# Optimization experiments

Measured on AMD Instinct MI355X. Metric: run time of the kernel, lower is better.

Reference implementation:

```python
import jax, jax.numpy as jnp
import numpy as np

B, P, F = 128, 196, 2048   # batch, num_pixels, feature_dim
E, H, V = 512, 512, 10000  # embed_dim, hidden_dim, vocab_size
T = 32                     # max caption length


def setup_inputs() -> dict:
    key = jax.random.key(0)
    ks = jax.random.split(key, 12)
    s_e, s_h, s_f = 1.0 / np.sqrt(E), 1.0 / np.sqrt(H), 1.0 / np.sqrt(F)
    return {
        "features": jax.random.normal(ks[0], (B, P, F), jnp.float32),
        "captions": jax.random.randint(ks[1], (B, T), 0, V),
        # embedding table (init uniform(-0.1, 0.1) in the original)
        "emb_W": jax.random.uniform(ks[2], (V, E), jnp.float32, -0.1, 0.1),
        # LSTMCell params (PyTorch layout: [4H, in] with gate order i,f,g,o)
        "W_ih": jax.random.uniform(ks[3], (4 * H, E), jnp.float32, -s_h, s_h),
        "W_hh": jax.random.uniform(ks[4], (4 * H, H), jnp.float32, -s_h, s_h),
        "b_ih": jax.random.uniform(ks[5], (4 * H,), jnp.float32, -s_h, s_h),
        "b_hh": jax.random.uniform(ks[6], (4 * H,), jnp.float32, -s_h, s_h),
        # init_h / init_c linear layers: feature_dim -> hidden_dim
        "Wh": jax.random.uniform(ks[7], (H, F), jnp.float32, -s_f, s_f),
        "bh": jax.random.uniform(ks[8], (H,), jnp.float32, -s_f, s_f),
        "Wc": jax.random.uniform(ks[9], (H, F), jnp.float32, -s_f, s_f),
        "bc": jax.random.uniform(ks[10], (H,), jnp.float32, -s_f, s_f),
        # output projection (uniform(-0.1, 0.1) weights, zero bias)
        "fc_W": jax.random.uniform(ks[11], (V, H), jnp.float32, -0.1, 0.1),
        "fc_b": jnp.zeros((V,), jnp.float32),
    }


def _decode(features, captions, emb_W, W_ih, W_hh, b_ih, b_hh, Wh, bh, Wc, bc, fc_W, fc_b):
    # init hidden state from mean pooled features
    mean_feat = features.mean(axis=1)                       # [B, F]
    h0 = mean_feat @ Wh.T + bh                              # [B, H]
    c0 = mean_feat @ Wc.T + bc                              # [B, H]

    embeds = emb_W[captions]                                # [B, T, E]
    # x-side gate preactivations for all steps at once: [T-1, B, 4H]
    x_gates = jnp.einsum('bte,ge->tbg', embeds[:, :-1, :], W_ih) + (b_ih + b_hh)

    def step(carry, xg):
        h, c = carry
        gates = xg + h @ W_hh.T                             # [B, 4H]
        i, f, g, o = jnp.split(gates, 4, axis=-1)
        i, f, o = jax.nn.sigmoid(i), jax.nn.sigmoid(f), jax.nn.sigmoid(o)
        g = jnp.tanh(g)
        c_new = f * c + i * g
        h_new = o * jnp.tanh(c_new)
        return (h_new, c_new), h_new

    _, hs = jax.lax.scan(step, (h0, c0), x_gates)           # hs: [T-1, B, H]
    hs = jnp.swapaxes(hs, 0, 1)                             # [B, T-1, H]
    # dropout is identity in eval mode; fc applied per step == batched matmul
    return jnp.einsum('bth,vh->btv', hs, fc_W) + fc_b       # [B, T-1, V]


def reference(features, captions, emb_W, W_ih, W_hh, b_ih, b_hh, Wh, bh, Wc, bc, fc_W, fc_b):
    return _decode(features, captions, emb_W, W_ih, W_hh, b_ih, b_hh, Wh, bh, Wc, bc, fc_W, fc_b)
```

## Files before the change

### kernel.cpp

```cpp
#include <hip/hip_runtime.h>
#include <hip/hip_bf16.h>
#include <cstddef>

#define Bz 128
#define Pz 196
#define Fz 2048
#define Ez 512
#define Hz 512
#define Vz 10000
#define Tz 32
#define TM 31
#define Mrows (Bz * TM)
#define MPAD 4096
#define G4 (4 * Hz)
#define NPAD 10240

typedef __attribute__((ext_vector_type(8))) short bf16x8;
typedef __attribute__((ext_vector_type(4))) float f32x4;

__device__ __forceinline__ void gload_lds16(const void* g, void* l) {
    __builtin_amdgcn_global_load_lds(
        (const __attribute__((address_space(1))) unsigned int*)g,
        (__attribute__((address_space(3))) unsigned int*)l, 16, 0, 0);
}
__device__ __forceinline__ ushort f2b(float x) {
    __hip_bfloat16 b = __float2bfloat16(x);
    return *reinterpret_cast<ushort*>(&b);
}
__device__ __forceinline__ float b2f(ushort u) {
    __hip_bfloat16 b = *reinterpret_cast<__hip_bfloat16*>(&u);
    return __bfloat162float(b);
}

__global__ __launch_bounds__(256) void meanpool(const float* __restrict__ feat,
                                                float* __restrict__ mean) {
    int idx = blockIdx.x * 256 + threadIdx.x;
    int b = idx >> 9;
    int q = idx & 511;
    const float4* base = reinterpret_cast<const float4*>(feat) +
                         (size_t)b * Pz * (Fz / 4) + q;
    float4 acc = {0.f, 0.f, 0.f, 0.f};
    for (int p = 0; p < Pz; ++p) {
        float4 v = base[(size_t)p * (Fz / 4)];
        acc.x += v.x; acc.y += v.y; acc.z += v.z; acc.w += v.w;
    }
    const float s = 1.0f / (float)Pz;
    acc.x *= s; acc.y *= s; acc.z *= s; acc.w *= s;
    reinterpret_cast<float4*>(mean)[idx] = acc;
}

#define PR0 (Mrows * 128)
#define PR1 (PR0 + 2 * G4 * 128)
#define PR2 (PR1 + NPAD * 128)
__global__ __launch_bounds__(256) void prep_all(
    const float* __restrict__ emb,  const int* __restrict__ cap,
    const float* __restrict__ Wih,  const float* __restrict__ Whh,
    const float* __restrict__ b1,   const float* __restrict__ b2,
    const float* __restrict__ fcW,
    ushort* __restrict__ embg, ushort* __restrict__ WihP,
    ushort* __restrict__ WhhP, float* __restrict__ bP,
    ushort* __restrict__ fcWb)
{
    int idx = blockIdx.x * 256 + threadIdx.x;
    if (idx < PR0) {
        int m = idx >> 7, kq = idx & 127;
        int b = m / TM;
        int t = m - b * TM;
        int row = cap[b * Tz + t];
        float4 v = reinterpret_cast<const float4*>(emb + (size_t)row * Ez)[kq];
        ushort4 o = {f2b(v.x), f2b(v.y), f2b(v.z), f2b(v.w)};
        reinterpret_cast<ushort4*>(embg + (size_t)m * Ez)[kq] = o;
    } else if (idx < PR1) {
        int rem = idx - PR0;
        int sel = rem >> 18;
        rem &= (1 << 18) - 1;
        int o = rem >> 7, kq = rem & 127;
        int j = o >> 2, g = o & 3;
        int in = g * Hz + j;
        if (sel == 0) {
            float4 v = reinterpret_cast<const float4*>(Wih + (size_t)in * Ez)[kq];
            ushort4 u = {f2b(v.x), f2b(v.y), f2b(v.z), f2b(v.w)};
            reinterpret_cast<ushort4*>(WihP + (size_t)o * Ez)[kq] = u;
            if (kq == 0) bP[o] = b1[in] + b2[in];
        } else {
            float4 v = reinterpret_cast<const float4*>(Whh + (size_t)in * Hz)[kq];
            ushort4 u = {f2b(v.x), f2b(v.y), f2b(v.z), f2b(v.w)};
            reinterpret_cast<ushort4*>(WhhP + (size_t)o * Hz)[kq] = u;
        }
    } else if (idx < PR2) {
        int i = idx - PR1;
        ushort4 o;
        if (i < Vz * Hz / 4) {
            float4 v = reinterpret_cast<const float4*>(fcW)[i];
            o.x = f2b(v.x); o.y = f2b(v.y); o.z = f2b(v.z); o.w = f2b(v.w);
        } else {
            o.x = o.y = o.z = o.w = 0;
        }
        reinterpret_cast<ushort4*>(fcWb)[i] = o;
    }
}

__global__ __launch_bounds__(256) void initk(
    const float* __restrict__ mean,
    const float* __restrict__ Wh, const float* __restrict__ Wc,
    float* __restrict__ partial)
{
    __shared__ float As[64][33];
    __shared__ float Bs2[64][33];
    const int n0 = blockIdx.x * 64;
    const int m0 = blockIdx.y * 64;
    const int kz = blockIdx.z;
    const int tid = threadIdx.x;
    const int tx = tid & 15, ty = tid >> 4;
    float acc[4][4] = {};

    for (int k0 = kz * 256; k0 < kz * 256 + 256; k0 += 32) {
#pragma unroll
        for (int i = 0; i < 2; ++i) {
            int e  = tid + i * 256;
            int r  = e >> 3;
            int cc = (e & 7) << 2;
            float4 va = *reinterpret_cast<const float4*>(
                mean + (size_t)(m0 + r) * Fz + k0 + cc);
            As[r][cc + 0] = va.x; As[r][cc + 1] = va.y;
            As[r][cc + 2] = va.z; As[r][cc + 3] = va.w;
            int n = n0 + r;
            const float* Brow = (n < Hz) ? (Wh + (size_t)n * Fz)
                                         : (Wc + (size_t)(n - Hz) * Fz);
            float4 vb = *reinterpret_cast<const float4*>(Brow + k0 + cc);
            Bs2[r][cc + 0] = vb.x; Bs2[r][cc + 1] = vb.y;
            Bs2[r][cc + 2] = vb.z; Bs2[r][cc + 3] = vb.w;
        }
        __syncthreads();
#pragma unroll
        for (int kk = 0; kk < 32; ++kk) {
            float a[4], bb[4];
#pragma unroll
            for (int i = 0; i < 4; ++i) a[i] = As[ty * 4 + i][kk];
#pragma unroll
            for (int j = 0; j < 4; ++j) bb[j] = Bs2[tx * 4 + j][kk];
#pragma unroll
            for (int i = 0; i < 4; ++i)
#pragma unroll
                for (int j = 0; j < 4; ++j)
                    acc[i][j] += a[i] * bb[j];
        }
        __syncthreads();
    }
#pragma unroll
    for (int i = 0; i < 4; ++i)
#pragma unroll
        for (int j = 0; j < 4; ++j)
            partial[((size_t)kz * 128 + m0 + ty * 4 + i) * 1024 + n0 + tx * 4 + j]
                = acc[i][j];
}

__global__ __launch_bounds__(256) void init_reduce(
    const float* __restrict__ partial,
    const float* __restrict__ bh, const float* __restrict__ bc,
    ushort* __restrict__ haHi, ushort* __restrict__ haLo,
    float* __restrict__ c0f)
{
    int idx = blockIdx.x * 256 + threadIdx.x;
    if (idx >= 128 * 1024) return;
    int m = idx >> 10, n = idx & 1023;
    float s = 0.f;
#pragma unroll
    for (int z = 0; z < 8; ++z)
        s += partial[((size_t)z * 128 + m) * 1024 + n];
    if (n < Hz) {
        s += bh[n];
        ushort hh = f2b(s);
        haHi[(size_t)m * Hz + n] = hh;
        haLo[(size_t)m * Hz + n] = f2b(s - b2f(hh));
    } else {
        c0f[(size_t)m * Hz + (n - Hz)] = s + bc[n - Hz];
    }
}

__global__ __launch_bounds__(256) void gemm_mfma(
    const ushort* __restrict__ A,
    const ushort* __restrict__ B,
    const float* __restrict__ bias,
    float* __restrict__ C,
    int Nb, int ldc, int K)
{
    __shared__ short Al[2][128 * 32];
    __shared__ short Bl[2][128 * 32];
    const int tid  = threadIdx.x;
    const int w    = tid >> 6;
    const int lane = tid & 63;

    const int nwg  = gridDim.x * gridDim.y;
    int orig = blockIdx.y * gridDim.x + blockIdx.x;
    int q = nwg >> 3, r = nwg & 7;
    int xcd = orig & 7, local = orig >> 3;
    int wgid = (xcd < r ? xcd * (q + 1) : r * (q + 1) + (xcd - r) * q) + local;
    const int m0 = (wgid / gridDim.x) * 128;
    const int n0 = (wgid % gridDim.x) * 128;
    const int wr = w >> 1, wc = w & 1;

    f32x4 acc[4][4] = {};

    const int srow = w * 32 + (lane >> 2);
    const int scol = (lane & 3) * 16;
    const char* Ag = (const char*)(A + (size_t)(m0 + srow) * K) + scol;
    const char* Bg = (const char*)(B + (size_t)(n0 + srow) * K) + scol;
    const size_t rstep = (size_t)16 * K * 2;
    const int ldsb = (w * 32) * 32;

    const int ko = (lane >> 4) * 8;
    const int fr = lane & 15;
    const int nk = K >> 5;

    gload_lds16(Ag,         Al[0] + ldsb);
    gload_lds16(Ag + rstep, Al[0] + ldsb + 16 * 32);
    gload_lds16(Bg,         Bl[0] + ldsb);
    gload_lds16(Bg + rstep, Bl[0] + ldsb + 16 * 32);
    __syncthreads();

    int cur = 0;
    for (int k = 0; k < nk; ++k) {
        if (k + 1 < nk) {
            const size_t kb = (size_t)(k + 1) * 64;
            gload_lds16(Ag + kb,         Al[cur ^ 1] + ldsb);
            gload_lds16(Ag + kb + rstep, Al[cur ^ 1] + ldsb + 16 * 32);
            gload_lds16(Bg + kb,         Bl[cur ^ 1] + ldsb);
            gload_lds16(Bg + kb + rstep, Bl[cur ^ 1] + ldsb + 16 * 32);
        }
        bf16x8 af[4], bf[4];
#pragma unroll
        for (int i = 0; i < 4; ++i)
            af[i] = *reinterpret_cast<const bf16x8*>(&Al[cur][(wr * 64 + i * 16 + fr) * 32 + ko]);
#pragma unroll
        for (int j = 0; j < 4; ++j)
            bf[j] = *reinterpret_cast<const bf16x8*>(&Bl[cur][(wc * 64 + j * 16 + fr) * 32 + ko]);
#pragma unroll
        for (int i = 0; i < 4; ++i)
#pragma unroll
            for (int j = 0; j < 4; ++j)
                acc[i][j] = __builtin_amdgcn_mfma_f32_16x16x32_bf16(
                    af[i], bf[j], acc[i][j], 0, 0, 0);
        __syncthreads();
        cur ^= 1;
    }

    const int r0 = (lane >> 4) * 4;
#pragma unroll
    for (int i = 0; i < 4; ++i) {
        int row = m0 + wr * 64 + i * 16 + r0;
#pragma unroll
        for (int j = 0; j < 4; ++j) {
            int col = n0 + wc * 64 + j * 16 + fr;
            if (col < Nb) {
                float bb = bias ? bias[col] : 0.f;
#pragma unroll
                for (int rr = 0; rr < 4; ++rr)
                    C[(size_t)(row + rr) * ldc + col] = acc[i][j][rr] + bb;
            }
        }
    }
}

__global__ __launch_bounds__(512) void fc8(
    const ushort* __restrict__ A,
    const ushort* __restrict__ B,
    const float* __restrict__ bias,
    float* __restrict__ C)
{
    __shared__ short Lds[4][2][256 * 32];

    const int tid  = threadIdx.x;
    const int w    = tid >> 6;
    const int lane = tid & 63;
    const int fr   = lane & 15;

    int orig = blockIdx.x;
    int wgid = (orig & 7) * 80 + (orig >> 3);
    const int m0 = (wgid / 40) * 256;
    const int n0 = (wgid % 40) * 256;
    const int wr = w >> 2, wc = w & 3;

    f32x4 acc[8][4] = {};

    const int sw16 = (((lane & 3) ^ ((lane >> 3) & 3)) << 4);
    const int srowA = lane >> 2;
    const int rsw = (((lane >> 4) ^ ((fr >> 1) & 3)) << 4);

#define FC_STAGE(T_) do {                                                     \
    const int b_ = (T_) & 3;                                                  \
    const size_t kb_ = (size_t)(T_) * 64;                                     \
    _Pragma("unroll")                                                         \
    for (int q_ = 0; q_ < 2; ++q_) {                                          \
        const int R_ = w * 32 + q_ * 16;                                      \
        gload_lds16((const char*)A + (size_t)(m0 + R_ + srowA) * 1024 + kb_ + sw16, \
                    (char*)&Lds[b_][0][0] + R_ * 64);                         \
        gload_lds16((const char*)B + (size_t)(n0 + R_ + srowA) * 1024 + kb_ + sw16, \
                    (char*)&Lds[b_][1][0] + R_ * 64);                         \
    }                                                                         \
} while (0)

#define FC_ITER(K_, VM_) do {                                                 \
    if ((K_) + 3 <= 15) FC_STAGE((K_) + 3);                                   \
    asm volatile("s_waitcnt vmcnt(" #VM_ ")" ::: "memory");                   \
    __builtin_amdgcn_s_barrier();                                             \
    __builtin_amdgcn_sched_barrier(0);                                        \
    const int b_ = (K_) & 3;                                                  \
    const char* Ab_ = (const char*)&Lds[b_][0][0];                            \
    const char* Bb_ = (const char*)&Lds[b_][1][0];                            \
    bf16x8 bfr_[4];                                                           \
    _Pragma("unroll")                                                         \
    for (int j_ = 0; j_ < 4; ++j_)                                            \
        bfr_[j_] = *reinterpret_cast<const bf16x8*>(                          \
            Bb_ + (wc * 64 + j_ * 16 + fr) * 64 + rsw);                       \
    bf16x8 afr_[8];                                                           \
    _Pragma("unroll")                                                         \
    for (int i_ = 0; i_ < 8; ++i_)                                            \
        afr_[i_] = *reinterpret_cast<const bf16x8*>(                          \
            Ab_ + (wr * 128 + i_ * 16 + fr) * 64 + rsw);                      \
    asm volatile("s_waitcnt lgkmcnt(0)" ::: "memory");                        \
    __builtin_amdgcn_sched_barrier(0);                                        \
    __builtin_amdgcn_s_barrier();                                             \
    __builtin_amdgcn_s_setprio(1);                                            \
    _Pragma("unroll")                                                         \
    for (int i_ = 0; i_ < 8; ++i_)                                            \
        _Pragma("unroll")                                                     \
        for (int j_ = 0; j_ < 4; ++j_)                                        \
            acc[i_][j_] = __builtin_amdgcn_mfma_f32_16x16x32_bf16(            \
                afr_[i_], bfr_[j_], acc[i_][j_], 0, 0, 0);                    \
    __builtin_amdgcn_s_setprio(0);                                            \
} while (0)

    FC_STAGE(0);
    FC_STAGE(1);
    FC_STAGE(2);

#pragma unroll 1
    for (int k = 0; k <= 12; ++k) {
        FC_ITER(k, 12);
    }
    FC_ITER(13, 8);
    FC_ITER(14, 4);
    FC_ITER(15, 0);

#undef FC_STAGE
#undef FC_ITER

    const int r0 = (lane >> 4) * 4;
#pragma unroll
    for (int i = 0; i < 8; ++i) {
        int row = m0 + wr * 128 + i * 16 + r0;
        if (row >= Mrows) continue;
#pragma unroll
        for (int j = 0; j < 4; ++j) {
            int col = n0 + wc * 64 + j * 16 + fr;
            if (col < Vz) {
                float bb = bias[col];
#pragma unroll
                for (int rr = 0; rr < 4; ++rr)
                    C[(size_t)(row + rr) * Vz + col] = acc[i][j][rr] + bb;
            }
        }
    }
}

__global__ __launch_bounds__(256) void lstm_step3(
    const float* __restrict__ xg,
    const ushort* __restrict__ Whi,
    const ushort* __restrict__ Ah,  const ushort* __restrict__ Alo,
    ushort* __restrict__ Oh, ushort* __restrict__ Ol,
    float* __restrict__ cst, ushort* __restrict__ hsb, int t)
{
    __shared__ float Cl[2][32][33];

    const int tid  = threadIdx.x;
    const int w    = tid >> 6;
    const int kh   = w >> 1;
    const int ch   = w & 1;
    const int lane = tid & 63;
    const int fr   = lane & 15;
    const int hi4  = lane >> 4;
    const int n0   = blockIdx.x * 32;
    const int j0   = blockIdx.x * 8;
    const int m0w  = blockIdx.y * 32;

    const int lm = tid >> 3;
    const int hq = tid & 7;
    const int em = m0w + lm;
    const int ej = j0 + hq;
    const float4 xv = *reinterpret_cast<const float4*>(
        xg + ((size_t)em * TM + t) * G4 + n0 + hq * 4);
    const float cold = cst[(size_t)em * Hz + ej];

    f32x4 acc[2] = {};
    const size_t kbase = (size_t)kh * 256;
    const ushort* Bp  = Whi + (size_t)(n0 + ch * 16 + fr) * Hz + kbase;
    const ushort* Ap0 = Ah  + (size_t)(m0w + fr) * Hz + kbase;
    const ushort* Ap1 = Ah  + (size_t)(m0w + 16 + fr) * Hz + kbase;
    const ushort* Lp0 = Alo + (size_t)(m0w + fr) * Hz + kbase;
    const ushort* Lp1 = Alo + (size_t)(m0w + 16 + fr) * Hz + kbase;

#pragma unroll
    for (int kc = 0; kc < 8; ++kc) {
        const size_t koff = (size_t)kc * 32 + hi4 * 8;
        bf16x8 bv  = *reinterpret_cast<const bf16x8*>(Bp  + koff);
        bf16x8 ah0 = *reinterpret_cast<const bf16x8*>(Ap0 + koff);
        bf16x8 ah1 = *reinterpret_cast<const bf16x8*>(Ap1 + koff);
        bf16x8 al0 = *reinterpret_cast<const bf16x8*>(Lp0 + koff);
        bf16x8 al1 = *reinterpret_cast<const bf16x8*>(Lp1 + koff);
        acc[0] = __builtin_amdgcn_mfma_f32_16x16x32_bf16(ah0, bv, acc[0], 0, 0, 0);
        acc[1] = __builtin_amdgcn_mfma_f32_16x16x32_bf16(ah1, bv, acc[1], 0, 0, 0);
        acc[0] = __builtin_amdgcn_mfma_f32_16x16x32_bf16(al0, bv, acc[0], 0, 0, 0);
        acc[1] = __builtin_amdgcn_mfma_f32_16x16x32_bf16(al1, bv, acc[1], 0, 0, 0);
    }

#pragma unroll
    for (int i = 0; i < 2; ++i)
#pragma unroll
        for (int r = 0; r < 4; ++r)
            Cl[kh][i * 16 + hi4 * 4 + r][ch * 16 + fr] = acc[i][r];
    __syncthreads();

    {
        const int bc = hq * 4;
        float gi = Cl[0][lm][bc + 0] + Cl[1][lm][bc + 0] + xv.x;
        float gf = Cl[0][lm][bc + 1] + Cl[1][lm][bc + 1] + xv.y;
        float gg = Cl[0][lm][bc + 2] + Cl[1][lm][bc + 2] + xv.z;
        float go = Cl[0][lm][bc + 3] + Cl[1][lm][bc + 3] + xv.w;

        float ig = 1.f / (1.f + expf(-gi));
        float fg = 1.f / (1.f + expf(-gf));
        float gt = tanhf(gg);
        float og = 1.f / (1.f + expf(-go));

        float cn = fg * cold + ig * gt;
        float hv = og * tanhf(cn);
        cst[(size_t)em * Hz + ej] = cn;

        ushort hh = f2b(hv);
        ushort hl = f2b(hv - b2f(hh));
        Oh[(size_t)em * Hz + ej] = hh;
        Ol[(size_t)em * Hz + ej] = hl;
        hsb[((size_t)em * TM + t) * Hz + ej] = hh;
    }
}

extern "C" void kernel_launch(void* const* d_in, const int* in_sizes, int n_in,
                              void* d_out, int out_size, void* d_ws, size_t ws_size,
                              hipStream_t stream) {
    const float* features = (const float*)d_in[0];
    const int*   captions = (const int*)d_in[1];
    const float* emb_W    = (const float*)d_in[2];
    const float* W_ih     = (const float*)d_in[3];
    const float* W_hh     = (const float*)d_in[4];
    const float* b_ih     = (const float*)d_in[5];
    const float* b_hh     = (const float*)d_in[6];
    const float* Wh       = (const float*)d_in[7];
    const float* bh       = (const float*)d_in[8];
    const float* Wc       = (const float*)d_in[9];
    const float* bc       = (const float*)d_in[10];
    const float* fc_W     = (const float*)d_in[11];
    const float* fc_b     = (const float*)d_in[12];
    float* out = (float*)d_out;

    float* w    = (float*)d_ws;
    float* mean = w;
    float* xg   = mean + Bz * Fz;
    float* partial = xg;
    float* c0f  = xg + (size_t)Mrows * G4;
    float* bP   = c0f + Bz * Hz;
    ushort* embg = (ushort*)(bP + G4);
    ushort* WihP = embg + (size_t)Mrows * Ez;
    ushort* Whi  = WihP + (size_t)G4 * Ez;
    ushort* fcWb = Whi + (size_t)G4 * Hz;
    ushort* hsb  = fcWb + (size_t)NPAD * Hz;
    ushort* haHi = hsb + (size_t)MPAD * Hz;
    ushort* haLo = haHi + Bz * Hz;
    ushort* hbHi = haLo + Bz * Hz;
    ushort* hbLo = hbHi + Bz * Hz;

    meanpool<<<(Bz * Fz / 4) / 256, 256, 0, stream>>>(features, mean);
    prep_all<<<(PR2 + 255) / 256, 256, 0, stream>>>(
        emb_W, captions, W_ih, W_hh, b_ih, b_hh, fc_W,
        embg, WihP, Whi, bP, fcWb);

    initk<<<dim3(16, 2, 8), 256, 0, stream>>>(mean, Wh, Wc, partial);
    init_reduce<<<(128 * 1024) / 256, 256, 0, stream>>>(
        partial, bh, bc, haHi, haLo, c0f);

    gemm_mfma<<<dim3(G4 / 128, Mrows / 128), 256, 0, stream>>>(
        embg, WihP, bP, xg, G4, G4, Ez);

    for (int t = 0; t < TM; ++t) {
        const ushort* ih = (t & 1) ? hbHi : haHi;
        const ushort* il = (t & 1) ? hbLo : haLo;
        ushort* oh = (t & 1) ? haHi : hbHi;
        ushort* ol = (t & 1) ? haLo : hbLo;
        lstm_step3<<<dim3(64, 4), 256, 0, stream>>>(
            xg, Whi, ih, il, oh, ol, c0f, hsb, t);
    }

    fc8<<<640, 512, 0, stream>>>(hsb, fcWb, fc_b, out);
}
```

Measured before the change: 423.2 us.

## Specialize x-gate GEMM with 4-stage LDS pipeline, swizzled LDS, and fixed shapes

Replaces the generic double-buffered bf16 MFMA GEMM for the input-side gate preactivations with a kernel specialised to K=512, N=2048. It uses a 4-deep global-to-LDS prefetch ring with explicit vmcnt waits, an XOR-swizzled LDS layout to avoid bank conflicts, setprio around the MFMA block, and a hardcoded XCD-aware workgroup mapping over a 1D grid of 496 blocks. The goal is to hide global-load latency and cut LDS bank conflicts in the x_gates GEMM. The cost is hardcoded shapes and more LDS use, which can lower occupancy. This GEMM is only a small part of the total pipeline.

```diff
diff --git a/kernel.cpp b/kernel.cpp
--- a/kernel.cpp
+++ b/kernel.cpp
@@ -178,72 +178,89 @@
     }
 }
 
-__global__ __launch_bounds__(256) void gemm_mfma(
+__global__ __launch_bounds__(256) void xg8(
     const ushort* __restrict__ A,
     const ushort* __restrict__ B,
     const float* __restrict__ bias,
-    float* __restrict__ C,
-    int Nb, int ldc, int K)
+    float* __restrict__ C)
 {
-    __shared__ short Al[2][128 * 32];
-    __shared__ short Bl[2][128 * 32];
+    __shared__ short Lds[4][2][128 * 32];
+
     const int tid  = threadIdx.x;
     const int w    = tid >> 6;
     const int lane = tid & 63;
-
-    const int nwg  = gridDim.x * gridDim.y;
-    int orig = blockIdx.y * gridDim.x + blockIdx.x;
-    int q = nwg >> 3, r = nwg & 7;
-    int xcd = orig & 7, local = orig >> 3;
-    int wgid = (xcd < r ? xcd * (q + 1) : r * (q + 1) + (xcd - r) * q) + local;
-    const int m0 = (wgid / gridDim.x) * 128;
-    const int n0 = (wgid % gridDim.x) * 128;
+    const int fr   = lane & 15;
+
+    int orig = blockIdx.x;
+    int wgid = (orig & 7) * 62 + (orig >> 3);
+    const int m0 = (wgid / 16) * 128;
+    const int n0 = (wgid % 16) * 128;
     const int wr = w >> 1, wc = w & 1;
 
     f32x4 acc[4][4] = {};
 
-    const int srow = w * 32 + (lane >> 2);
-    const int scol = (lane & 3) * 16;
-    const char* Ag = (const char*)(A + (size_t)(m0 + srow) * K) + scol;
-    const char* Bg = (const char*)(B + (size_t)(n0 + srow) * K) + scol;
-    const size_t rstep = (size_t)16 * K * 2;
-    const int ldsb = (w * 32) * 32;
-
-    const int ko = (lane >> 4) * 8;
-    const int fr = lane & 15;
-    const int nk = K >> 5;
-
-    gload_lds16(Ag,         Al[0] + ldsb);
-    gload_lds16(Ag + rstep, Al[0] + ldsb + 16 * 32);
-    gload_lds16(Bg,         Bl[0] + ldsb);
-    gload_lds16(Bg + rstep, Bl[0] + ldsb + 16 * 32);
-    __syncthreads();
-
-    int cur = 0;
-    for (int k = 0; k < nk; ++k) {
-        if (k + 1 < nk) {
-            const size_t kb = (size_t)(k + 1) * 64;
-            gload_lds16(Ag + kb,         Al[cur ^ 1] + ldsb);
-            gload_lds16(Ag + kb + rstep, Al[cur ^ 1] + ldsb + 16 * 32);
-            gload_lds16(Bg + kb,         Bl[cur ^ 1] + ldsb);
-            gload_lds16(Bg + kb + rstep, Bl[cur ^ 1] + ldsb + 16 * 32);
-        }
-        bf16x8 af[4], bf[4];
-#pragma unroll
-        for (int i = 0; i < 4; ++i)
-            af[i] = *reinterpret_cast<const bf16x8*>(&Al[cur][(wr * 64 + i * 16 + fr) * 32 + ko]);
-#pragma unroll
-        for (int j = 0; j < 4; ++j)
-            bf[j] = *reinterpret_cast<const bf16x8*>(&Bl[cur][(wc * 64 + j * 16 + fr) * 32 + ko]);
-#pragma unroll
-        for (int i = 0; i < 4; ++i)
-#pragma unroll
-            for (int j = 0; j < 4; ++j)
-                acc[i][j] = __builtin_amdgcn_mfma_f32_16x16x32_bf16(
-                    af[i], bf[j], acc[i][j], 0, 0, 0);
-        __syncthreads();
-        cur ^= 1;
-    }
+    const int sw16 = (((lane & 3) ^ ((lane >> 3) & 3)) << 4);
+    const int srowA = lane >> 2;
+    const int rsw = (((lane >> 4) ^ ((fr >> 1) & 3)) << 4);
+
+#define XG_STAGE(T_) do {                                                     \
+    const int b_ = (T_) & 3;                                                  \
+    const size_t kb_ = (size_t)(T_) * 64;                                     \
+    _Pragma("unroll")                                                         \
+    for (int q_ = 0; q_ < 2; ++q_) {                                          \
+        const int R_ = w * 32 + q_ * 16;                                      \
+        gload_lds16((const char*)A + (size_t)(m0 + R_ + srowA) * 1024 + kb_ + sw16, \
+                    (char*)&Lds[b_][0][0] + R_ * 64);                         \
+        gload_lds16((const char*)B + (size_t)(n0 + R_ + srowA) * 1024 + kb_ + sw16, \
+                    (char*)&Lds[b_][1][0] + R_ * 64);                         \
+    }                                                                         \
+} while (0)
+
+#define XG_ITER(K_, VM_) do {                                                 \
+    if ((K_) + 3 <= 15) XG_STAGE((K_) + 3);                                   \
+    asm volatile("s_waitcnt vmcnt(" #VM_ ")" ::: "memory");                   \
+    __builtin_amdgcn_s_barrier();                                             \
+    __builtin_amdgcn_sched_barrier(0);                                        \
+    const int b_ = (K_) & 3;                                                  \
+    const char* Ab_ = (const char*)&Lds[b_][0][0];                            \
+    const char* Bb_ = (const char*)&Lds[b_][1][0];                            \
+    bf16x8 bfr_[4];                                                           \
+    _Pragma("unroll")                                                         \
+    for (int j_ = 0; j_ < 4; ++j_)                                            \
+        bfr_[j_] = *reinterpret_cast<const bf16x8*>(                          \
+            Bb_ + (wc * 64 + j_ * 16 + fr) * 64 + rsw);                       \
+    bf16x8 afr_[4];                                                           \
+    _Pragma("unroll")                                                         \
+    for (int i_ = 0; i_ < 4; ++i_)                                            \
+        afr_[i_] = *reinterpret_cast<const bf16x8*>(                          \
+            Ab_ + (wr * 64 + i_ * 16 + fr) * 64 + rsw);                       \
+    asm volatile("s_waitcnt lgkmcnt(0)" ::: "memory");                        \
+    __builtin_amdgcn_sched_barrier(0);                                        \
+    __builtin_amdgcn_s_barrier();                                             \
+    __builtin_amdgcn_s_setprio(1);                                            \
+    _Pragma("unroll")                                                         \
+    for (int i_ = 0; i_ < 4; ++i_)                                            \
+        _Pragma("unroll")                                                     \
+        for (int j_ = 0; j_ < 4; ++j_)                                        \
+            acc[i_][j_] = __builtin_amdgcn_mfma_f32_16x16x32_bf16(            \
+                afr_[i_], bfr_[j_], acc[i_][j_], 0, 0, 0);                    \
+    __builtin_amdgcn_s_setprio(0);                                            \
+} while (0)
+
+    XG_STAGE(0);
+    XG_STAGE(1);
+    XG_STAGE(2);
+
+#pragma unroll 1
+    for (int k = 0; k <= 12; ++k) {
+        XG_ITER(k, 12);
+    }
+    XG_ITER(13, 8);
+    XG_ITER(14, 4);
+    XG_ITER(15, 0);
+
+#undef XG_STAGE
+#undef XG_ITER
 
     const int r0 = (lane >> 4) * 4;
 #pragma unroll
@@ -252,12 +269,10 @@
 #pragma unroll
         for (int j = 0; j < 4; ++j) {
             int col = n0 + wc * 64 + j * 16 + fr;
-            if (col < Nb) {
-                float bb = bias ? bias[col] : 0.f;
-#pragma unroll
-                for (int rr = 0; rr < 4; ++rr)
-                    C[(size_t)(row + rr) * ldc + col] = acc[i][j][rr] + bb;
-            }
+            float bb = bias[col];
+#pragma unroll
+            for (int rr = 0; rr < 4; ++rr)
+                C[(size_t)(row + rr) * G4 + col] = acc[i][j][rr] + bb;
         }
     }
 }
@@ -488,8 +503,7 @@
     init_reduce<<<(128 * 1024) / 256, 256, 0, stream>>>(
         partial, bh, bc, haHi, haLo, c0f);
 
-    gemm_mfma<<<dim3(G4 / 128, Mrows / 128), 256, 0, stream>>>(
-        embg, WihP, bP, xg, G4, G4, Ez);
+    xg8<<<496, 256, 0, stream>>>(embg, WihP, bP, xg);
 
     for (int t = 0; t < TM; ++t) {
         const ushort* ih = (t & 1) ? hbHi : haHi;
```

Result: no change. 417.4 us (-1.4%).
